# Kernel optimization log

Measured on AMD Instinct MI355X. Metric: run time of the kernel, lower is better.

## Reference

```python
import jax, jax.numpy as jnp
import numpy as np

BSZ, D = 256, 512
LOGIT_SCALE = 1.0


def setup_inputs() -> dict:
    key = jax.random.key(0)
    k1, k2, k3 = jax.random.split(key, 3)
    x = jax.random.normal(k1, (BSZ, D), dtype=jnp.float32)
    y = jax.random.normal(k2, (BSZ, D), dtype=jnp.float32)
    z = jax.random.normal(k3, (BSZ, D), dtype=jnp.float32)
    return {"x": x, "y": y, "z": z}


def _logits_n_squared(anchor, a, b, shift):
    # torch recursion: products[i*bsz + r] = a[r] * roll(b, i)[r] = a[r] * b[(r - i) % bsz]
    bsz = anchor.shape[0]
    P = a[None, :, :] * b[shift]              # (i, r, d) = (bsz, bsz, d)
    logits = jnp.einsum('ad,ird->air', anchor, P)  # (a, i, r)
    return LOGIT_SCALE * logits.reshape(bsz, bsz * bsz)


def _cross_entropy_diag(logits):
    bsz = logits.shape[0]
    lp = jax.nn.log_softmax(logits, axis=-1)
    idx = jnp.arange(bsz)
    return -jnp.mean(lp[idx, idx])


def reference(x, y, z):
    bsz = x.shape[0]
    r = jnp.arange(bsz)
    shift = (r[None, :] - r[:, None]) % bsz   # (i, r): index into b after roll by i
    reps = [x, y, z]
    losses = []
    for i in range(3):
        anchor = reps[i]
        non_anchor = [reps[j] for j in range(3) if j != i]
        logits = _logits_n_squared(anchor, non_anchor[0], non_anchor[1], shift)
        losses.append(_cross_entropy_diag(logits))
    return sum(losses) / 3.0
```

## Files before the change

kernel.cpp:

```cpp
#include <hip/hip_runtime.h>

#define DIM 512
#define BK 32
#define ASTRIDE 40

typedef unsigned int uint;
typedef unsigned short ushort;
typedef __attribute__((ext_vector_type(8))) short short8;
typedef __attribute__((ext_vector_type(4))) float f32x4;

#define GLOAD_LDS(g, l) __builtin_amdgcn_global_load_lds( \
    (const __attribute__((address_space(1))) void*)(g), \
    (__attribute__((address_space(3))) void*)(l), 16, 0, 0)

__device__ __forceinline__ uint pack_bf16(float a, float b) {
    union { float f; uint u; } ua, ub;
    ua.f = a; ub.f = b;
    uint x0 = ua.u + 0x8000u;
    uint x1 = ub.u + 0x8000u;
    return __builtin_amdgcn_perm(x1, x0, 0x07060302);
}

__global__ void zconv_kernel(const float* __restrict__ z, ushort* __restrict__ zb) {
    int t = blockIdx.x * 256 + threadIdx.x;
    int f = t * 8;
    float4 a = *(const float4*)(z + f);
    float4 b = *(const float4*)(z + f + 4);
    uint4 o;
    o.x = pack_bf16(a.x, a.y);
    o.y = pack_bf16(a.z, a.w);
    o.z = pack_bf16(b.x, b.y);
    o.w = pack_bf16(b.z, b.w);
    *(uint4*)(zb + f) = o;
}

__global__ void __launch_bounds__(512, 4)
gemm_fused(const float* __restrict__ x, const float* __restrict__ y,
           const ushort* __restrict__ zb, const float* __restrict__ z,
           float* __restrict__ rowM, float* __restrict__ rowS,
           float* __restrict__ colM, float* __restrict__ colS,
           float* __restrict__ diag, uint* __restrict__ counter) {
    __shared__ __align__(16) float xs[DIM];
    __shared__ __align__(16) ushort As[2][128 * ASTRIDE];
    __shared__ __align__(16) ushort Bs[2][256 * BK];
    __shared__ float redA[128 * 4];
    __shared__ float rowMaxS[128];
    __shared__ float redB[256 * 2];
    __shared__ float colMaxS[256];
    __shared__ float dred[8];

    const int tid = threadIdx.x;
    const int a   = blockIdx.x >> 1;
    const int rt  = blockIdx.x & 1;

    if (blockIdx.x == 0 && tid == 0) *counter = 0u;

    xs[tid] = x[a * DIM + tid];

    const int lane = tid & 63;
    const int wave = tid >> 6;
    const int quad = lane >> 4;
    const int ln15 = lane & 15;
    const int wr = wave >> 2;
    const int wc = wave & 3;

    if (rt == 0) {
        float p = xs[tid] * y[a * DIM + tid] * z[a * DIM + tid];
        #pragma unroll
        for (int m = 1; m < 64; m <<= 1) p += __shfl_xor(p, m, 64);
        if (lane == 0) dred[wave] = p;
        __syncthreads();
        if (tid == 0) {
            float s = 0.f;
            #pragma unroll
            for (int w2 = 0; w2 < 8; ++w2) s += dred[w2];
            diag[a] = s;
        }
    }
    __syncthreads();

    f32x4 acc[4][4];
    #pragma unroll
    for (int i = 0; i < 4; ++i)
        #pragma unroll
        for (int j = 0; j < 4; ++j)
            acc[i][j] = (f32x4){0.f, 0.f, 0.f, 0.f};

    const int rA = tid >> 2;
    const int kA = (tid & 3) * 8;
    const float* yrow = y + (rt * 128 + rA) * DIM + kA;

    const int s0 = wave * 128 + lane;
    const int row0 = s0 >> 2, kc0 = ((s0 & 3) - (row0 >> 1)) & 3;
    const ushort* gB0 = zb + row0 * DIM + kc0 * 8;
    const int s1 = s0 + 64;
    const int row1 = s1 >> 2, kc1 = ((s1 & 3) - (row1 >> 1)) & 3;
    const ushort* gB1 = zb + row1 * DIM + kc1 * 8;

    GLOAD_LDS(gB0, &Bs[0][wave * 1024]);
    GLOAD_LDS(gB1, &Bs[0][wave * 1024 + 512]);
    float4 ya = *(const float4*)(yrow);
    float4 yb = *(const float4*)(yrow + 4);
    {
        float4 x0 = *(const float4*)(xs + kA);
        float4 x1 = *(const float4*)(xs + kA + 4);
        uint4 o;
        o.x = pack_bf16(ya.x * x0.x, ya.y * x0.y);
        o.y = pack_bf16(ya.z * x0.z, ya.w * x0.w);
        o.z = pack_bf16(yb.x * x1.x, yb.y * x1.y);
        o.w = pack_bf16(yb.z * x1.z, yb.w * x1.w);
        *(uint4*)(&As[0][rA * ASTRIDE + kA]) = o;
    }
    ya = *(const float4*)(yrow + 32);
    yb = *(const float4*)(yrow + 36);

    #pragma unroll 2
    for (int kt = 0; kt < 16; ++kt) {
        const int cur = kt & 1, nxt = cur ^ 1;
        __syncthreads();
        if (kt < 15) {
            GLOAD_LDS(gB0 + (kt + 1) * 32, &Bs[nxt][wave * 1024]);
            GLOAD_LDS(gB1 + (kt + 1) * 32, &Bs[nxt][wave * 1024 + 512]);
        }
        short8 af[4], bfr[4];
        #pragma unroll
        for (int i = 0; i < 4; ++i)
            af[i] = *(const short8*)(&As[cur][(wr * 64 + i * 16 + ln15) * ASTRIDE + quad * 8]);
        #pragma unroll
        for (int j = 0; j < 4; ++j) {
            int row = wc * 64 + j * 16 + ln15;
            int pos = row * 4 + ((quad + (row >> 1)) & 3);
            bfr[j] = *(const short8*)(&Bs[cur][pos * 8]);
        }
        #pragma unroll
        for (int i = 0; i < 4; ++i)
            #pragma unroll
            for (int j = 0; j < 4; ++j)
                acc[i][j] = __builtin_amdgcn_mfma_f32_16x16x32_bf16(af[i], bfr[j], acc[i][j], 0, 0, 0);
        if (kt < 15) {
            const int k1 = (kt + 1) * 32;
            float4 x0 = *(const float4*)(xs + k1 + kA);
            float4 x1 = *(const float4*)(xs + k1 + kA + 4);
            uint4 o;
            o.x = pack_bf16(ya.x * x0.x, ya.y * x0.y);
            o.y = pack_bf16(ya.z * x0.z, ya.w * x0.w);
            o.z = pack_bf16(yb.x * x1.x, yb.y * x1.y);
            o.w = pack_bf16(yb.z * x1.z, yb.w * x1.w);
            *(uint4*)(&As[nxt][rA * ASTRIDE + kA]) = o;
            if (kt < 14) {
                ya = *(const float4*)(yrow + (kt + 2) * 32);
                yb = *(const float4*)(yrow + (kt + 2) * 32 + 4);
            }
        }
    }
    __syncthreads();

    #pragma unroll
    for (int i = 0; i < 4; ++i) {
        #pragma unroll
        for (int reg = 0; reg < 4; ++reg) {
            float m = fmaxf(fmaxf(acc[i][0][reg], acc[i][1][reg]),
                            fmaxf(acc[i][2][reg], acc[i][3][reg]));
            #pragma unroll
            for (int d = 1; d < 16; d <<= 1) m = fmaxf(m, __shfl_xor(m, d, 64));
            if (ln15 == 0) redA[(wr * 64 + i * 16 + quad * 4 + reg) * 4 + wc] = m;
        }
    }
    __syncthreads();
    if (tid < 128) {
        float m = fmaxf(fmaxf(redA[tid * 4 + 0], redA[tid * 4 + 1]),
                        fmaxf(redA[tid * 4 + 2], redA[tid * 4 + 3]));
        rowMaxS[tid] = m;
    }
    __syncthreads();
    #pragma unroll
    for (int i = 0; i < 4; ++i) {
        #pragma unroll
        for (int reg = 0; reg < 4; ++reg) {
            int r = wr * 64 + i * 16 + quad * 4 + reg;
            float rm = rowMaxS[r];
            float s = __expf(acc[i][0][reg] - rm) + __expf(acc[i][1][reg] - rm)
                    + __expf(acc[i][2][reg] - rm) + __expf(acc[i][3][reg] - rm);
            #pragma unroll
            for (int d = 1; d < 16; d <<= 1) s += __shfl_xor(s, d, 64);
            if (ln15 == 0) redA[r * 4 + wc] = s;
        }
    }
    __syncthreads();
    if (tid < 128) {
        float s = redA[tid * 4 + 0] + redA[tid * 4 + 1] + redA[tid * 4 + 2] + redA[tid * 4 + 3];
        int rg = rt * 128 + tid;
        rowM[a * 256 + rg] = rowMaxS[tid];
        rowS[a * 256 + rg] = s;
    }

    #pragma unroll
    for (int j = 0; j < 4; ++j) {
        float m = -3.4e38f;
        #pragma unroll
        for (int i = 0; i < 4; ++i)
            #pragma unroll
            for (int reg = 0; reg < 4; ++reg)
                m = fmaxf(m, acc[i][j][reg]);
        m = fmaxf(m, __shfl_xor(m, 16, 64));
        m = fmaxf(m, __shfl_xor(m, 32, 64));
        if (quad == 0) redB[(wc * 64 + j * 16 + ln15) * 2 + wr] = m;
    }
    __syncthreads();
    if (tid < 256) colMaxS[tid] = fmaxf(redB[tid * 2], redB[tid * 2 + 1]);
    __syncthreads();
    #pragma unroll
    for (int j = 0; j < 4; ++j) {
        int n = wc * 64 + j * 16 + ln15;
        float cm = colMaxS[n];
        float s = 0.f;
        #pragma unroll
        for (int i = 0; i < 4; ++i)
            #pragma unroll
            for (int reg = 0; reg < 4; ++reg)
                s += __expf(acc[i][j][reg] - cm);
        s += __shfl_xor(s, 16, 64);
        s += __shfl_xor(s, 32, 64);
        if (quad == 0) redB[n * 2 + wr] = s;
    }
    __syncthreads();
    if (tid < 256) {
        float s = redB[tid * 2] + redB[tid * 2 + 1];
        colM[(a * 256 + tid) * 2 + rt] = colMaxS[tid];
        colS[(a * 256 + tid) * 2 + rt] = s;
    }
}

__device__ __forceinline__ float blk_max(float v, float* sm) {
    #pragma unroll
    for (int d = 1; d < 64; d <<= 1) v = fmaxf(v, __shfl_xor(v, d, 64));
    __syncthreads();
    if ((threadIdx.x & 63) == 0) sm[threadIdx.x >> 6] = v;
    __syncthreads();
    return fmaxf(fmaxf(sm[0], sm[1]), fmaxf(sm[2], sm[3]));
}
__device__ __forceinline__ float blk_sum(float v, float* sm) {
    #pragma unroll
    for (int d = 1; d < 64; d <<= 1) v += __shfl_xor(v, d, 64);
    __syncthreads();
    if ((threadIdx.x & 63) == 0) sm[threadIdx.x >> 6] = v;
    __syncthreads();
    return sm[0] + sm[1] + sm[2] + sm[3];
}

__global__ void combine_final(const float* __restrict__ rowM, const float* __restrict__ rowS,
                              const float* __restrict__ colM, const float* __restrict__ colS,
                              const float* __restrict__ diag,
                              float* __restrict__ m123, uint* __restrict__ counter,
                              float* __restrict__ out) {
    __shared__ float sm[4];
    __shared__ uint isLast;
    int b = blockIdx.x, t = threadIdx.x;
    float m = rowM[b * 256 + t], s = rowS[b * 256 + t];
    float M = blk_max(m, sm);
    float S = blk_sum(s * __expf(m - M), sm);
    float M1 = M + __logf(S);
    m = rowM[t * 256 + b]; s = rowS[t * 256 + b];
    M = blk_max(m, sm);
    S = blk_sum(s * __expf(m - M), sm);
    float M2 = M + __logf(S);
    float am = colM[(t * 256 + b) * 2 + 0], av = colS[(t * 256 + b) * 2 + 0];
    float bm = colM[(t * 256 + b) * 2 + 1], bv = colS[(t * 256 + b) * 2 + 1];
    m = fmaxf(am, bm);
    s = av * __expf(am - m) + bv * __expf(bm - m);
    M = blk_max(m, sm);
    S = blk_sum(s * __expf(m - M), sm);
    float M3 = M + __logf(S);
    if (t == 0) {
        m123[b] = M1 + M2 + M3;
        __threadfence();
        isLast = (atomicAdd(counter, 1u) == 255u) ? 1u : 0u;
    }
    __syncthreads();
    if (isLast) {
        __threadfence();
        const volatile float* vm = (const volatile float*)m123;
        const volatile float* vd = (const volatile float*)diag;
        float S1 = blk_sum(vm[t], sm);
        float S2 = blk_sum(vd[t], sm);
        if (t == 0) out[0] = S1 / 768.0f - S2 / 256.0f;
    }
}

extern "C" void kernel_launch(void* const* d_in, const int* in_sizes, int n_in,
                              void* d_out, int out_size, void* d_ws, size_t ws_size,
                              hipStream_t stream) {
    const float* x = (const float*)d_in[0];
    const float* y = (const float*)d_in[1];
    const float* z = (const float*)d_in[2];
    char* w = (char*)d_ws;
    ushort* zb  = (ushort*)(w);
    float* rowM = (float*)(w + 262144);
    float* rowS = (float*)(w + 524288);
    float* colM = (float*)(w + 786432);
    float* colS = (float*)(w + 1310720);
    float* diag = (float*)(w + 1835008);
    float* m123 = (float*)(w + 1836032);
    uint*  counter = (uint*)(w + 1837056);
    float* out  = (float*)d_out;

    zconv_kernel<<<64, 256, 0, stream>>>(z, zb);
    gemm_fused<<<512, 512, 0, stream>>>(x, y, zb, z, rowM, rowS, colM, colS, diag, counter);
    combine_final<<<256, 256, 0, stream>>>(rowM, rowS, colM, colS, diag, m123, counter, out);
}
```

Before: 98.77 us.

## Split each anchor's GEMM into four 64-row tiles across 1024 blocks

Each fused GEMM block now handles 64 rows of the y-product tile instead of 128, which doubles the grid to 1024 blocks and halves the per-thread accumulator count. Column partial max/sum statistics are now stored as four partials per column, and combine_final merges them online. MFMA sections are wrapped in s_setprio to favour the compute waves. The aim is better occupancy and load balance across CUs. The cost is that every block reloads the full z tile from bf16 memory, so B traffic doubles, and there are more partials to reduce.

```diff
diff --git a/kernel.cpp b/kernel.cpp
--- a/kernel.cpp
+++ b/kernel.cpp
@@ -41,17 +41,17 @@
            float* __restrict__ colM, float* __restrict__ colS,
            float* __restrict__ diag, uint* __restrict__ counter) {
     __shared__ __align__(16) float xs[DIM];
-    __shared__ __align__(16) ushort As[2][128 * ASTRIDE];
+    __shared__ __align__(16) ushort As[2][64 * ASTRIDE];
     __shared__ __align__(16) ushort Bs[2][256 * BK];
-    __shared__ float redA[128 * 4];
-    __shared__ float rowMaxS[128];
+    __shared__ float redA[64 * 4];
+    __shared__ float rowMaxS[64];
     __shared__ float redB[256 * 2];
     __shared__ float colMaxS[256];
     __shared__ float dred[8];
 
     const int tid = threadIdx.x;
-    const int a   = blockIdx.x >> 1;
-    const int rt  = blockIdx.x & 1;
+    const int a   = blockIdx.x >> 2;
+    const int q   = blockIdx.x & 3;
 
     if (blockIdx.x == 0 && tid == 0) *counter = 0u;
 
@@ -64,7 +64,7 @@
     const int wr = wave >> 2;
     const int wc = wave & 3;
 
-    if (rt == 0) {
+    if (q == 0) {
         float p = xs[tid] * y[a * DIM + tid] * z[a * DIM + tid];
         #pragma unroll
         for (int m = 1; m < 64; m <<= 1) p += __shfl_xor(p, m, 64);
@@ -79,16 +79,16 @@
     }
     __syncthreads();
 
-    f32x4 acc[4][4];
-    #pragma unroll
-    for (int i = 0; i < 4; ++i)
+    f32x4 acc[2][4];
+    #pragma unroll
+    for (int i = 0; i < 2; ++i)
         #pragma unroll
         for (int j = 0; j < 4; ++j)
             acc[i][j] = (f32x4){0.f, 0.f, 0.f, 0.f};
 
-    const int rA = tid >> 2;
-    const int kA = (tid & 3) * 8;
-    const float* yrow = y + (rt * 128 + rA) * DIM + kA;
+    const int rA = tid >> 3;
+    const int kA = (tid & 7) * 4;
+    const float* yrow = y + (q * 64 + rA) * DIM + kA;
 
     const int s0 = wave * 128 + lane;
     const int row0 = s0 >> 2, kc0 = ((s0 & 3) - (row0 >> 1)) & 3;
@@ -100,19 +100,14 @@
     GLOAD_LDS(gB0, &Bs[0][wave * 1024]);
     GLOAD_LDS(gB1, &Bs[0][wave * 1024 + 512]);
     float4 ya = *(const float4*)(yrow);
-    float4 yb = *(const float4*)(yrow + 4);
     {
         float4 x0 = *(const float4*)(xs + kA);
-        float4 x1 = *(const float4*)(xs + kA + 4);
-        uint4 o;
+        uint2 o;
         o.x = pack_bf16(ya.x * x0.x, ya.y * x0.y);
         o.y = pack_bf16(ya.z * x0.z, ya.w * x0.w);
-        o.z = pack_bf16(yb.x * x1.x, yb.y * x1.y);
-        o.w = pack_bf16(yb.z * x1.z, yb.w * x1.w);
-        *(uint4*)(&As[0][rA * ASTRIDE + kA]) = o;
+        *(uint2*)(&As[0][rA * ASTRIDE + kA]) = o;
     }
     ya = *(const float4*)(yrow + 32);
-    yb = *(const float4*)(yrow + 36);
 
     #pragma unroll 2
     for (int kt = 0; kt < 16; ++kt) {
@@ -122,62 +117,59 @@
             GLOAD_LDS(gB0 + (kt + 1) * 32, &Bs[nxt][wave * 1024]);
             GLOAD_LDS(gB1 + (kt + 1) * 32, &Bs[nxt][wave * 1024 + 512]);
         }
-        short8 af[4], bfr[4];
-        #pragma unroll
-        for (int i = 0; i < 4; ++i)
-            af[i] = *(const short8*)(&As[cur][(wr * 64 + i * 16 + ln15) * ASTRIDE + quad * 8]);
+        short8 bfr[4];
         #pragma unroll
         for (int j = 0; j < 4; ++j) {
             int row = wc * 64 + j * 16 + ln15;
             int pos = row * 4 + ((quad + (row >> 1)) & 3);
             bfr[j] = *(const short8*)(&Bs[cur][pos * 8]);
         }
-        #pragma unroll
-        for (int i = 0; i < 4; ++i)
+        __builtin_amdgcn_s_setprio(1);
+        #pragma unroll
+        for (int i = 0; i < 2; ++i) {
+            short8 af = *(const short8*)(&As[cur][(wr * 32 + i * 16 + ln15) * ASTRIDE + quad * 8]);
             #pragma unroll
             for (int j = 0; j < 4; ++j)
-                acc[i][j] = __builtin_amdgcn_mfma_f32_16x16x32_bf16(af[i], bfr[j], acc[i][j], 0, 0, 0);
+                acc[i][j] = __builtin_amdgcn_mfma_f32_16x16x32_bf16(af, bfr[j], acc[i][j], 0, 0, 0);
+        }
+        __builtin_amdgcn_s_setprio(0);
         if (kt < 15) {
             const int k1 = (kt + 1) * 32;
             float4 x0 = *(const float4*)(xs + k1 + kA);
-            float4 x1 = *(const float4*)(xs + k1 + kA + 4);
-            uint4 o;
+            uint2 o;
             o.x = pack_bf16(ya.x * x0.x, ya.y * x0.y);
             o.y = pack_bf16(ya.z * x0.z, ya.w * x0.w);
-            o.z = pack_bf16(yb.x * x1.x, yb.y * x1.y);
-            o.w = pack_bf16(yb.z * x1.z, yb.w * x1.w);
-            *(uint4*)(&As[nxt][rA * ASTRIDE + kA]) = o;
+            *(uint2*)(&As[nxt][rA * ASTRIDE + kA]) = o;
             if (kt < 14) {
                 ya = *(const float4*)(yrow + (kt + 2) * 32);
-                yb = *(const float4*)(yrow + (kt + 2) * 32 + 4);
             }
         }
     }
     __syncthreads();
 
     #pragma unroll
-    for (int i = 0; i < 4; ++i) {
+    for (int i = 0; i < 2; ++i) {
         #pragma unroll
         for (int reg = 0; reg < 4; ++reg) {
             float m = fmaxf(fmaxf(acc[i][0][reg], acc[i][1][reg]),
                             fmaxf(acc[i][2][reg], acc[i][3][reg]));
             #pragma unroll
             for (int d = 1; d < 16; d <<= 1) m = fmaxf(m, __shfl_xor(m, d, 64));
-            if (ln15 == 0) redA[(wr * 64 + i * 16 + quad * 4 + reg) * 4 + wc] = m;
-        }
-    }
-    __syncthreads();
-    if (tid < 128) {
+            if (ln15 == 0) redA[(wr * 32 + i * 16 + quad * 4 + reg) * 4 + wc] = m;
+        }
+    }
+    __syncthreads();
+    if (tid < 64) {
         float m = fmaxf(fmaxf(redA[tid * 4 + 0], redA[tid * 4 + 1]),
                         fmaxf(redA[tid * 4 + 2], redA[tid * 4 + 3]));
         rowMaxS[tid] = m;
     }
     __syncthreads();
     #pragma unroll
-    for (int i = 0; i < 4; ++i) {
+    for (int i = 0; i < 2; ++i) {
         #pragma unroll
         for (int reg = 0; reg < 4; ++reg) {
-            int r = wr * 64 + i * 16 + quad * 4 + reg;
+            int r = wr * 32 + i * 16 + quad * 4 + reg;
             float rm = rowMaxS[r];
             float s = __expf(acc[i][0][reg] - rm) + __expf(acc[i][1][reg] - rm)
                     + __expf(acc[i][2][reg] - rm) + __expf(acc[i][3][reg] - rm);
@@ -187,9 +179,9 @@
         }
     }
     __syncthreads();
-    if (tid < 128) {
+    if (tid < 64) {
         float s = redA[tid * 4 + 0] + redA[tid * 4 + 1] + redA[tid * 4 + 2] + redA[tid * 4 + 3];
-        int rg = rt * 128 + tid;
+        int rg = q * 64 + tid;
         rowM[a * 256 + rg] = rowMaxS[tid];
         rowS[a * 256 + rg] = s;
     }
@@ -198,7 +190,7 @@
     for (int j = 0; j < 4; ++j) {
         float m = -3.4e38f;
         #pragma unroll
-        for (int i = 0; i < 4; ++i)
+        for (int i = 0; i < 2; ++i)
             #pragma unroll
             for (int reg = 0; reg < 4; ++reg)
                 m = fmaxf(m, acc[i][j][reg]);
@@ -215,7 +207,7 @@
         float cm = colMaxS[n];
         float s = 0.f;
         #pragma unroll
-        for (int i = 0; i < 4; ++i)
+        for (int i = 0; i < 2; ++i)
             #pragma unroll
             for (int reg = 0; reg < 4; ++reg)
                 s += __expf(acc[i][j][reg] - cm);
@@ -226,8 +218,8 @@
     __syncthreads();
     if (tid < 256) {
         float s = redB[tid * 2] + redB[tid * 2 + 1];
-        colM[(a * 256 + tid) * 2 + rt] = colMaxS[tid];
-        colS[(a * 256 + tid) * 2 + rt] = s;
+        colM[(a * 256 + tid) * 4 + q] = colMaxS[tid];
+        colS[(a * 256 + tid) * 4 + q] = s;
     }
 }
 
@@ -264,10 +256,16 @@
     M = blk_max(m, sm);
     S = blk_sum(s * __expf(m - M), sm);
     float M2 = M + __logf(S);
-    float am = colM[(t * 256 + b) * 2 + 0], av = colS[(t * 256 + b) * 2 + 0];
-    float bm = colM[(t * 256 + b) * 2 + 1], bv = colS[(t * 256 + b) * 2 + 1];
-    m = fmaxf(am, bm);
-    s = av * __expf(am - m) + bv * __expf(bm - m);
+    m = colM[(t * 256 + b) * 4 + 0];
+    s = colS[(t * 256 + b) * 4 + 0];
+    #pragma unroll
+    for (int qq = 1; qq < 4; ++qq) {
+        float m2 = colM[(t * 256 + b) * 4 + qq];
+        float s2 = colS[(t * 256 + b) * 4 + qq];
+        float mm = fmaxf(m, m2);
+        s = s * __expf(m - mm) + s2 * __expf(m2 - mm);
+        m = mm;
+    }
     M = blk_max(m, sm);
     S = blk_sum(s * __expf(m - M), sm);
     float M3 = M + __logf(S);
@@ -298,13 +296,13 @@
     float* rowM = (float*)(w + 262144);
     float* rowS = (float*)(w + 524288);
     float* colM = (float*)(w + 786432);
-    float* colS = (float*)(w + 1310720);
-    float* diag = (float*)(w + 1835008);
-    float* m123 = (float*)(w + 1836032);
-    uint*  counter = (uint*)(w + 1837056);
+    float* colS = (float*)(w + 1835008);
+    float* diag = (float*)(w + 2883584);
+    float* m123 = (float*)(w + 2884608);
+    uint*  counter = (uint*)(w + 2885632);
     float* out  = (float*)d_out;
 
     zconv_kernel<<<64, 256, 0, stream>>>(z, zb);
-    gemm_fused<<<512, 512, 0, stream>>>(x, y, zb, z, rowM, rowS, colM, colS, diag, counter);
+    gemm_fused<<<1024, 512, 0, stream>>>(x, y, zb, z, rowM, rowS, colM, colS, diag, counter);
     combine_final<<<256, 256, 0, stream>>>(rowM, rowS, colM, colS, diag, m123, counter, out);
 }
```

After: 110.4 us. 1.12x slower.

## Triple-buffer B tiles with prefetch distance two and manual waitcnt barriers

Applied to the files above, without the earlier changes.

The GEMM main loop moves from a double-buffered B tile to a three-slot ring with global-to-LDS loads issued two iterations ahead. The per-iteration __syncthreads is replaced by an explicit s_waitcnt vmcnt(2) plus s_barrier, so the newest prefetch can stay in flight. The y loads for the A operand are reordered and fenced with sched_barrier. The z conversion kernel also uses half the work per thread across twice as many blocks. This adds LDS use, which may lower occupancy, and the hand-written waitcnt counts carry correctness risk if the compiler emits other vector memory ops.

```diff
diff --git a/kernel.cpp b/kernel.cpp
--- a/kernel.cpp
+++ b/kernel.cpp
@@ -1,7 +1,6 @@
 #include <hip/hip_runtime.h>
 
 #define DIM 512
-#define BK 32
 #define ASTRIDE 40
 
 typedef unsigned int uint;
@@ -23,15 +22,12 @@
 
 __global__ void zconv_kernel(const float* __restrict__ z, ushort* __restrict__ zb) {
     int t = blockIdx.x * 256 + threadIdx.x;
-    int f = t * 8;
+    int f = t * 4;
     float4 a = *(const float4*)(z + f);
-    float4 b = *(const float4*)(z + f + 4);
-    uint4 o;
+    uint2 o;
     o.x = pack_bf16(a.x, a.y);
     o.y = pack_bf16(a.z, a.w);
-    o.z = pack_bf16(b.x, b.y);
-    o.w = pack_bf16(b.z, b.w);
-    *(uint4*)(zb + f) = o;
+    *(uint2*)(zb + f) = o;
 }
 
 __global__ void __launch_bounds__(512, 4)
@@ -42,7 +38,7 @@
            float* __restrict__ diag, uint* __restrict__ counter) {
     __shared__ __align__(16) float xs[DIM];
     __shared__ __align__(16) ushort As[2][128 * ASTRIDE];
-    __shared__ __align__(16) ushort Bs[2][256 * BK];
+    __shared__ __align__(16) ushort Bs[3][256 * 32];
     __shared__ float redA[128 * 4];
     __shared__ float rowMaxS[128];
     __shared__ float redB[256 * 2];
@@ -97,10 +93,13 @@
     const int row1 = s1 >> 2, kc1 = ((s1 & 3) - (row1 >> 1)) & 3;
     const ushort* gB1 = zb + row1 * DIM + kc1 * 8;
 
+    float4 ya = *(const float4*)(yrow);
+    float4 yb = *(const float4*)(yrow + 4);
+    __builtin_amdgcn_sched_barrier(0);
     GLOAD_LDS(gB0, &Bs[0][wave * 1024]);
     GLOAD_LDS(gB1, &Bs[0][wave * 1024 + 512]);
-    float4 ya = *(const float4*)(yrow);
-    float4 yb = *(const float4*)(yrow + 4);
+    GLOAD_LDS(gB0 + 32, &Bs[1][wave * 1024]);
+    GLOAD_LDS(gB1 + 32, &Bs[1][wave * 1024 + 512]);
     {
         float4 x0 = *(const float4*)(xs + kA);
         float4 x1 = *(const float4*)(xs + kA + 4);
@@ -111,26 +110,30 @@
         o.w = pack_bf16(yb.z * x1.z, yb.w * x1.w);
         *(uint4*)(&As[0][rA * ASTRIDE + kA]) = o;
     }
-    ya = *(const float4*)(yrow + 32);
-    yb = *(const float4*)(yrow + 36);
-
-    #pragma unroll 2
+    asm volatile("s_waitcnt vmcnt(2) lgkmcnt(0)" ::: "memory");
+    __builtin_amdgcn_s_barrier();
+    __builtin_amdgcn_sched_barrier(0);
+
+    int biCur = 0, biN2 = 2;
     for (int kt = 0; kt < 16; ++kt) {
-        const int cur = kt & 1, nxt = cur ^ 1;
-        __syncthreads();
         if (kt < 15) {
-            GLOAD_LDS(gB0 + (kt + 1) * 32, &Bs[nxt][wave * 1024]);
-            GLOAD_LDS(gB1 + (kt + 1) * 32, &Bs[nxt][wave * 1024 + 512]);
+            ya = *(const float4*)(yrow + (kt + 1) * 32);
+            yb = *(const float4*)(yrow + (kt + 1) * 32 + 4);
+        }
+        __builtin_amdgcn_sched_barrier(0);
+        if (kt < 14) {
+            GLOAD_LDS(gB0 + (kt + 2) * 32, &Bs[biN2][wave * 1024]);
+            GLOAD_LDS(gB1 + (kt + 2) * 32, &Bs[biN2][wave * 1024 + 512]);
         }
         short8 af[4], bfr[4];
         #pragma unroll
         for (int i = 0; i < 4; ++i)
-            af[i] = *(const short8*)(&As[cur][(wr * 64 + i * 16 + ln15) * ASTRIDE + quad * 8]);
+            af[i] = *(const short8*)(&As[kt & 1][(wr * 64 + i * 16 + ln15) * ASTRIDE + quad * 8]);
         #pragma unroll
         for (int j = 0; j < 4; ++j) {
             int row = wc * 64 + j * 16 + ln15;
             int pos = row * 4 + ((quad + (row >> 1)) & 3);
-            bfr[j] = *(const short8*)(&Bs[cur][pos * 8]);
+            bfr[j] = *(const short8*)(&Bs[biCur][pos * 8]);
         }
         #pragma unroll
         for (int i = 0; i < 4; ++i)
@@ -146,12 +149,13 @@
             o.y = pack_bf16(ya.z * x0.z, ya.w * x0.w);
             o.z = pack_bf16(yb.x * x1.x, yb.y * x1.y);
             o.w = pack_bf16(yb.z * x1.z, yb.w * x1.w);
-            *(uint4*)(&As[nxt][rA * ASTRIDE + kA]) = o;
-            if (kt < 14) {
-                ya = *(const float4*)(yrow + (kt + 2) * 32);
-                yb = *(const float4*)(yrow + (kt + 2) * 32 + 4);
-            }
-        }
+            *(uint4*)(&As[(kt + 1) & 1][rA * ASTRIDE + kA]) = o;
+        }
+        asm volatile("s_waitcnt vmcnt(2) lgkmcnt(0)" ::: "memory");
+        __builtin_amdgcn_s_barrier();
+        __builtin_amdgcn_sched_barrier(0);
+        int tmp = biCur; biCur = biCur + 1 == 3 ? 0 : biCur + 1;
+        biN2 = biN2 + 1 == 3 ? 0 : biN2 + 1; (void)tmp;
     }
     __syncthreads();
 
@@ -304,7 +308,7 @@
     uint*  counter = (uint*)(w + 1837056);
     float* out  = (float*)d_out;
 
-    zconv_kernel<<<64, 256, 0, stream>>>(z, zb);
+    zconv_kernel<<<128, 256, 0, stream>>>(z, zb);
     gemm_fused<<<512, 512, 0, stream>>>(x, y, zb, z, rowM, rowS, colM, colS, diag, counter);
     combine_final<<<256, 256, 0, stream>>>(rowM, rowS, colM, colS, diag, m123, counter, out);
 }
```

Result: no change. 98.75 us (-0.0%).
